# Optimization experiments

Hardware: AMD Instinct MI355X
Metric: run time of the kernel (lower is better)

## Reference

```python
import jax, jax.numpy as jnp
import numpy as np
from jax import lax

BN_EPS = 1e-5


def setup_inputs() -> dict:
    key = jax.random.key(0)
    k = jax.random.split(key, 7)
    B, H, W = 128, 224, 224
    return {
        "x": jax.random.normal(k[0], (B, 1, H, W), dtype=jnp.float32),
        "conv_w": jax.random.normal(k[1], (16, 1, 5, 5), dtype=jnp.float32) * 0.1,
        "conv_b": jax.random.normal(k[2], (16,), dtype=jnp.float32) * 0.1,
        "gamma": jax.random.uniform(k[3], (16,), dtype=jnp.float32, minval=0.5, maxval=1.5),
        "beta": jax.random.normal(k[4], (16,), dtype=jnp.float32) * 0.1,
        "run_mean": jax.random.normal(k[5], (16,), dtype=jnp.float32) * 0.1,
        "run_var": jax.random.uniform(k[6], (16,), dtype=jnp.float32, minval=0.5, maxval=1.5),
    }


def reference(x, conv_w, conv_b, gamma, beta, run_mean, run_var):
    # Conv2d(1,16,5,stride=1,padding=2): NCHW x OIHW -> NCHW
    y = lax.conv_general_dilated(
        x, conv_w, window_strides=(1, 1), padding=[(2, 2), (2, 2)],
        dimension_numbers=("NCHW", "OIHW", "NCHW"))
    y = y + conv_b[None, :, None, None]
    # BatchNorm2d(16) in inference form with running stats
    scale = gamma * lax.rsqrt(run_var + BN_EPS)
    y = y * scale[None, :, None, None] + (beta - run_mean * scale)[None, :, None, None]
    # ReLU
    y = jnp.maximum(y, 0.0)
    # MaxPool2d(kernel=2, stride=2)
    out = lax.reduce_window(y, -jnp.inf, lax.max,
                            window_dimensions=(1, 1, 2, 2),
                            window_strides=(1, 1, 2, 2),
                            padding="VALID")
    return out  # [B, 16, H/2, W/2]
```

## Files before the change

kernel.cpp:

```cpp
#include <hip/hip_runtime.h>
#include <stdint.h>

#define IMG 224
#define OUT_DIM 112
#define NCH 16

typedef __fp16 half2_t __attribute__((ext_vector_type(2)));
typedef __fp16 half8_t __attribute__((ext_vector_type(8)));
typedef float floatx4 __attribute__((ext_vector_type(4)));

#define WS_WTAB 32

__global__ void prep_kernel(const float* __restrict__ conv_w,
                            const float* __restrict__ conv_b,
                            const float* __restrict__ gamma,
                            const float* __restrict__ beta,
                            const float* __restrict__ run_mean,
                            const float* __restrict__ run_var,
                            uint32_t* __restrict__ ws)
{
    int ch = threadIdx.x;
    if (ch >= NCH) return;
    float s = gamma[ch] * rsqrtf(run_var[ch] + 1e-5f);
    float t = fmaf(s, conv_b[ch] - run_mean[ch], beta[ch]);
    ((float2*)ws)[ch] = make_float2(s, t);

    const float* w = conv_w + ch * 25;
    uint32_t* wt = ws + WS_WTAB + ch * 16;
    for (int d = 0; d < 16; ++d) {
        float v[2];
        for (int e = 0; e < 2; ++e) {
            int k = 2 * d + e;
            int r = k / 6, c = k - 6 * r;
            v[e] = (k < 30 && c < 5) ? w[r * 5 + c] : 0.f;
        }
        half2_t h = __builtin_amdgcn_cvt_pkrtz(v[0], v[1]);
        wt[d] = __builtin_bit_cast(uint32_t, h);
    }
}

__device__ __forceinline__ uint32_t imc_addr(uint32_t P, uint32_t q) {
    return (P >> 1) * 128u + ((((P & 1u) << 2) | q) ^ ((P >> 1) & 7u)) * 16u;
}

__global__ __launch_bounds__(256)
void conv_mfma(const float* __restrict__ x,
               const uint32_t* __restrict__ ws,
               float* __restrict__ out)
{
    __shared__ uint32_t imc[16384];

    const int tid = threadIdx.x;
    const int bx = blockIdx.x, by = blockIdx.y, b = blockIdx.z;
    const float* xb = x + (size_t)b * IMG * IMG;

    const int px = tid & 15, py = tid >> 4;
    const int gy0 = by * 32 + 2 * py - 2;
    const int gx0 = bx * 32 + 2 * px - 2;

    float f[6][8];
    if (bx >= 1 && bx <= 5 && by >= 1 && by <= 5) {
        #pragma unroll
        for (int r = 0; r < 6; ++r) {
            const float* rowp = xb + (gy0 + r) * IMG + gx0;
            #pragma unroll
            for (int j = 0; j < 4; ++j) {
                float2 v = *(const float2*)(rowp + 2 * j);
                f[r][2 * j] = v.x; f[r][2 * j + 1] = v.y;
            }
        }
    } else {
        #pragma unroll
        for (int r = 0; r < 6; ++r) {
            int gy = gy0 + r;
            #pragma unroll
            for (int j = 0; j < 8; ++j) {
                int gx = gx0 + j;
                f[r][j] = ((unsigned)gy < IMG && (unsigned)gx < IMG)
                        ? xb[gy * IMG + gx] : 0.f;
            }
        }
    }

    uint32_t pr[6][6];
    #pragma unroll
    for (int r = 0; r < 6; ++r) {
        pr[r][0] = __builtin_bit_cast(uint32_t, __builtin_amdgcn_cvt_pkrtz(f[r][0], f[r][1]));
        pr[r][1] = __builtin_bit_cast(uint32_t, __builtin_amdgcn_cvt_pkrtz(f[r][2], f[r][3]));
        pr[r][2] = __builtin_bit_cast(uint32_t, __builtin_amdgcn_cvt_pkrtz(f[r][4], f[r][5]));
        pr[r][3] = __builtin_bit_cast(uint32_t, __builtin_amdgcn_cvt_pkrtz(f[r][1], f[r][2]));
        pr[r][4] = __builtin_bit_cast(uint32_t, __builtin_amdgcn_cvt_pkrtz(f[r][3], f[r][4]));
        pr[r][5] = __builtin_bit_cast(uint32_t, __builtin_amdgcn_cvt_pkrtz(f[r][5], f[r][6]));
    }

    #pragma unroll
    for (int dy = 0; dy < 2; ++dy) {
        #pragma unroll
        for (int dx = 0; dx < 2; ++dx) {
            const uint32_t P = (2 * py + dy) * 32 + 2 * px + dx;
            const int o = 3 * dx;
            uint4 c0 = {pr[dy  ][o], pr[dy  ][o+1], pr[dy  ][o+2], pr[dy+1][o]};
            uint4 c1 = {pr[dy+1][o+1], pr[dy+1][o+2], pr[dy+2][o], pr[dy+2][o+1]};
            uint4 c2 = {pr[dy+2][o+2], pr[dy+3][o], pr[dy+3][o+1], pr[dy+3][o+2]};
            uint4 c3 = {pr[dy+4][o], pr[dy+4][o+1], pr[dy+4][o+2], 0u};
            *(uint4*)((char*)imc + imc_addr(P, 0)) = c0;
            *(uint4*)((char*)imc + imc_addr(P, 1)) = c1;
            *(uint4*)((char*)imc + imc_addr(P, 2)) = c2;
            *(uint4*)((char*)imc + imc_addr(P, 3)) = c3;
        }
    }

    const int lane = tid & 63;
    const int n = lane & 15;
    const int q = lane >> 4;
    uint4 bw = ((const uint4*)(ws + WS_WTAB))[n * 4 + q];
    half8_t bfrag = __builtin_bit_cast(half8_t, bw);
    float2 st = ((const float2*)ws)[n];

    __syncthreads();

    const int w = tid >> 6;
    float* outb = out + (size_t)b * NCH * (OUT_DIM * OUT_DIM)
                      + (size_t)n * (OUT_DIM * OUT_DIM);

    #pragma unroll
    for (int i = 0; i < 8; ++i) {
        const int gp = w * 8 + i;
        const int Y = gp >> 1, xh = gp & 1;
        const uint32_t P0 = 64u * Y + 16u * xh + (uint32_t)n;
        uint4 a0w = *(const uint4*)((const char*)imc + imc_addr(P0, q));
        uint4 a1w = *(const uint4*)((const char*)imc + imc_addr(P0 + 32u, q));
        floatx4 z = {0.f, 0.f, 0.f, 0.f};
        floatx4 d0 = __builtin_amdgcn_mfma_f32_16x16x32_f16(
            __builtin_bit_cast(half8_t, a0w), bfrag, z, 0, 0, 0);
        floatx4 d1 = __builtin_amdgcn_mfma_f32_16x16x32_f16(
            __builtin_bit_cast(half8_t, a1w), bfrag, z, 0, 0, 0);
        float c0 = fmaxf(d0[0], d1[0]);
        float c1 = fmaxf(d0[1], d1[1]);
        float c2 = fmaxf(d0[2], d1[2]);
        float c3 = fmaxf(d0[3], d1[3]);
        float o0 = fmaxf(fmaf(fmaxf(c0, c1), st.x, st.y), 0.f);
        float o1 = fmaxf(fmaf(fmaxf(c2, c3), st.x, st.y), 0.f);
        const int gyp = by * 16 + Y;
        const int gxp = bx * 16 + xh * 8 + 2 * q;
        *(float2*)(outb + gyp * OUT_DIM + gxp) = make_float2(o0, o1);
    }
}

extern "C" void kernel_launch(void* const* d_in, const int* in_sizes, int n_in,
                              void* d_out, int out_size, void* d_ws, size_t ws_size,
                              hipStream_t stream) {
    const float* x        = (const float*)d_in[0];
    const float* conv_w   = (const float*)d_in[1];
    const float* conv_b   = (const float*)d_in[2];
    const float* gamma    = (const float*)d_in[3];
    const float* beta     = (const float*)d_in[4];
    const float* run_mean = (const float*)d_in[5];
    const float* run_var  = (const float*)d_in[6];
    float* out = (float*)d_out;
    uint32_t* ws = (uint32_t*)d_ws;

    prep_kernel<<<1, 64, 0, stream>>>(conv_w, conv_b, gamma, beta, run_mean, run_var, ws);

    dim3 grid(7, 7, 128);
    dim3 block(256);
    conv_mfma<<<grid, block, 0, stream>>>(x, ws, out);
}
```

Measured before the change: 183.4 us.

## Halve per-block row tile to cut LDS and registers for higher occupancy

Each block now covers 16 input rows instead of 32, and each thread builds im2col rows for one input row (even and odd columns) instead of a 2x2 patch. This halves shared memory to 32KB and shrinks per-thread register arrays, so more blocks can be resident per CU and latency hiding improves. The grid doubles in y. The cost is more halo rows re-read from global memory across blocks, plus more block launches. The weight-packing code in the prep kernel is rewritten but produces the same layout.

```diff
diff --git a/kernel.cpp b/kernel.cpp
--- a/kernel.cpp
+++ b/kernel.cpp
@@ -28,13 +28,13 @@
     const float* w = conv_w + ch * 25;
     uint32_t* wt = ws + WS_WTAB + ch * 16;
     for (int d = 0; d < 16; ++d) {
-        float v[2];
-        for (int e = 0; e < 2; ++e) {
-            int k = 2 * d + e;
-            int r = k / 6, c = k - 6 * r;
-            v[e] = (k < 30 && c < 5) ? w[r * 5 + c] : 0.f;
+        float v0 = 0.f, v1 = 0.f;
+        if (d < 15) {
+            int r = d / 3, j = d - 3 * r;
+            if (j < 2) { v0 = w[r * 5 + 2 * j]; v1 = w[r * 5 + 2 * j + 1]; }
+            else       { v0 = w[r * 5 + 4]; }
         }
-        half2_t h = __builtin_amdgcn_cvt_pkrtz(v[0], v[1]);
+        half2_t h = __builtin_amdgcn_cvt_pkrtz(v0, v1);
         wt[d] = __builtin_bit_cast(uint32_t, h);
     }
 }
@@ -43,38 +43,43 @@
     return (P >> 1) * 128u + ((((P & 1u) << 2) | q) ^ ((P >> 1) & 7u)) * 16u;
 }
 
+__device__ __forceinline__ uint32_t pk(float a, float b) {
+    return __builtin_bit_cast(uint32_t, __builtin_amdgcn_cvt_pkrtz(a, b));
+}
+
 __global__ __launch_bounds__(256)
 void conv_mfma(const float* __restrict__ x,
                const uint32_t* __restrict__ ws,
                float* __restrict__ out)
 {
-    __shared__ uint32_t imc[16384];
+    __shared__ uint32_t imc[8192];
 
     const int tid = threadIdx.x;
     const int bx = blockIdx.x, by = blockIdx.y, b = blockIdx.z;
     const float* xb = x + (size_t)b * IMG * IMG;
 
-    const int px = tid & 15, py = tid >> 4;
-    const int gy0 = by * 32 + 2 * py - 2;
+    const int px = tid & 15;
+    const int cy = tid >> 4;
     const int gx0 = bx * 32 + 2 * px - 2;
+    const int gy0 = by * 16 + cy - 2;
 
-    float f[6][8];
-    if (bx >= 1 && bx <= 5 && by >= 1 && by <= 5) {
+    float f[5][6];
+    if (bx >= 1 && bx <= 5 && by >= 1 && by <= 12) {
         #pragma unroll
-        for (int r = 0; r < 6; ++r) {
+        for (int r = 0; r < 5; ++r) {
             const float* rowp = xb + (gy0 + r) * IMG + gx0;
             #pragma unroll
-            for (int j = 0; j < 4; ++j) {
+            for (int j = 0; j < 3; ++j) {
                 float2 v = *(const float2*)(rowp + 2 * j);
                 f[r][2 * j] = v.x; f[r][2 * j + 1] = v.y;
             }
         }
     } else {
         #pragma unroll
-        for (int r = 0; r < 6; ++r) {
+        for (int r = 0; r < 5; ++r) {
             int gy = gy0 + r;
             #pragma unroll
-            for (int j = 0; j < 8; ++j) {
+            for (int j = 0; j < 6; ++j) {
                 int gx = gx0 + j;
                 f[r][j] = ((unsigned)gy < IMG && (unsigned)gx < IMG)
                         ? xb[gy * IMG + gx] : 0.f;
@@ -82,32 +87,37 @@
         }
     }
 
-    uint32_t pr[6][6];
+    uint32_t e[5][3], o[5][3];
     #pragma unroll
-    for (int r = 0; r < 6; ++r) {
-        pr[r][0] = __builtin_bit_cast(uint32_t, __builtin_amdgcn_cvt_pkrtz(f[r][0], f[r][1]));
-        pr[r][1] = __builtin_bit_cast(uint32_t, __builtin_amdgcn_cvt_pkrtz(f[r][2], f[r][3]));
-        pr[r][2] = __builtin_bit_cast(uint32_t, __builtin_amdgcn_cvt_pkrtz(f[r][4], f[r][5]));
-        pr[r][3] = __builtin_bit_cast(uint32_t, __builtin_amdgcn_cvt_pkrtz(f[r][1], f[r][2]));
-        pr[r][4] = __builtin_bit_cast(uint32_t, __builtin_amdgcn_cvt_pkrtz(f[r][3], f[r][4]));
-        pr[r][5] = __builtin_bit_cast(uint32_t, __builtin_amdgcn_cvt_pkrtz(f[r][5], f[r][6]));
+    for (int r = 0; r < 5; ++r) {
+        e[r][0] = pk(f[r][0], f[r][1]);
+        e[r][1] = pk(f[r][2], f[r][3]);
+        e[r][2] = pk(f[r][4], f[r][5]);
+        o[r][0] = pk(f[r][1], f[r][2]);
+        o[r][1] = pk(f[r][3], f[r][4]);
+        o[r][2] = pk(f[r][5], f[r][5]);
     }
 
-    #pragma unroll
-    for (int dy = 0; dy < 2; ++dy) {
-        #pragma unroll
-        for (int dx = 0; dx < 2; ++dx) {
-            const uint32_t P = (2 * py + dy) * 32 + 2 * px + dx;
-            const int o = 3 * dx;
-            uint4 c0 = {pr[dy  ][o], pr[dy  ][o+1], pr[dy  ][o+2], pr[dy+1][o]};
-            uint4 c1 = {pr[dy+1][o+1], pr[dy+1][o+2], pr[dy+2][o], pr[dy+2][o+1]};
-            uint4 c2 = {pr[dy+2][o+2], pr[dy+3][o], pr[dy+3][o+1], pr[dy+3][o+2]};
-            uint4 c3 = {pr[dy+4][o], pr[dy+4][o+1], pr[dy+4][o+2], 0u};
-            *(uint4*)((char*)imc + imc_addr(P, 0)) = c0;
-            *(uint4*)((char*)imc + imc_addr(P, 1)) = c1;
-            *(uint4*)((char*)imc + imc_addr(P, 2)) = c2;
-            *(uint4*)((char*)imc + imc_addr(P, 3)) = c3;
-        }
+    const uint32_t Pe = (uint32_t)(cy * 32 + 2 * px);
+    {
+        uint4 c0 = {e[0][0], e[0][1], e[0][2], e[1][0]};
+        uint4 c1 = {e[1][1], e[1][2], e[2][0], e[2][1]};
+        uint4 c2 = {e[2][2], e[3][0], e[3][1], e[3][2]};
+        uint4 c3 = {e[4][0], e[4][1], e[4][2], 0u};
+        *(uint4*)((char*)imc + imc_addr(Pe, 0)) = c0;
+        *(uint4*)((char*)imc + imc_addr(Pe, 1)) = c1;
+        *(uint4*)((char*)imc + imc_addr(Pe, 2)) = c2;
+        *(uint4*)((char*)imc + imc_addr(Pe, 3)) = c3;
+    }
+    {
+        uint4 c0 = {o[0][0], o[0][1], o[0][2], o[1][0]};
+        uint4 c1 = {o[1][1], o[1][2], o[2][0], o[2][1]};
+        uint4 c2 = {o[2][2], o[3][0], o[3][1], o[3][2]};
+        uint4 c3 = {o[4][0], o[4][1], o[4][2], 0u};
+        *(uint4*)((char*)imc + imc_addr(Pe + 1, 0)) = c0;
+        *(uint4*)((char*)imc + imc_addr(Pe + 1, 1)) = c1;
+        *(uint4*)((char*)imc + imc_addr(Pe + 1, 2)) = c2;
+        *(uint4*)((char*)imc + imc_addr(Pe + 1, 3)) = c3;
     }
 
     const int lane = tid & 63;
@@ -124,8 +134,8 @@
                       + (size_t)n * (OUT_DIM * OUT_DIM);
 
     #pragma unroll
-    for (int i = 0; i < 8; ++i) {
-        const int gp = w * 8 + i;
+    for (int i = 0; i < 4; ++i) {
+        const int gp = w * 4 + i;
         const int Y = gp >> 1, xh = gp & 1;
         const uint32_t P0 = 64u * Y + 16u * xh + (uint32_t)n;
         uint4 a0w = *(const uint4*)((const char*)imc + imc_addr(P0, q));
@@ -141,7 +151,7 @@
         float c3 = fmaxf(d0[3], d1[3]);
         float o0 = fmaxf(fmaf(fmaxf(c0, c1), st.x, st.y), 0.f);
         float o1 = fmaxf(fmaf(fmaxf(c2, c3), st.x, st.y), 0.f);
-        const int gyp = by * 16 + Y;
+        const int gyp = by * 8 + Y;
         const int gxp = bx * 16 + xh * 8 + 2 * q;
         *(float2*)(outb + gyp * OUT_DIM + gxp) = make_float2(o0, o1);
     }
@@ -162,7 +172,7 @@
 
     prep_kernel<<<1, 64, 0, stream>>>(conv_w, conv_b, gamma, beta, run_mean, run_var, ws);
 
-    dim3 grid(7, 7, 128);
+    dim3 grid(7, 14, 128);
     dim3 block(256);
     conv_mfma<<<grid, block, 0, stream>>>(x, ws, out);
 }
```

Result: slower. 189.5 us (+3.3%).
